# Optimization experiments

Hardware: AMD Instinct MI355X
Metric: run time of the kernel (lower is better)

## Reference

```python
import jax, jax.numpy as jnp
import numpy as np

E, N, R, OUT = 8, 4096, 128, 4096


def setup_inputs() -> dict:
    key = jax.random.key(0)
    kx, kw = jax.random.split(key)
    # x: stacked list of per-expert inputs, x[i] has shape [N, r]
    x = jax.random.normal(kx, (E, N, R), dtype=jnp.float32)
    # W: per-expert nn.Linear weights, torch layout [out_features, in_features]
    W = jax.random.normal(kw, (E, OUT, R), dtype=jnp.float32) * (1.0 / np.sqrt(R))
    return {"x": x, "W": W}


def reference(x, W):
    # Grouped GEMM over experts: out[e] = x[e] @ W[e].T  (Linear, no bias)
    # x: [E, N, r], W: [E, out, r] -> out: [E, N, out]
    return jnp.einsum("enr,eor->eno", x, W)
```

## Files before the change

### kernel.cpp

```cpp
#include <hip/hip_runtime.h>
#include <hip/hip_bf16.h>


#define NEXP 8
#define NROW 4096
#define KD   128
#define NOUT 4096
#define TILE 128

typedef __attribute__((ext_vector_type(8))) short bf16x8;
typedef __attribute__((ext_vector_type(4))) float f32x4;

__device__ __forceinline__ unsigned int pack2_bf16(float lo, float hi) {
  unsigned int ulo = __float_as_uint(lo);
  ulo += 0x7fffu + ((ulo >> 16) & 1u);
  unsigned int uhi = __float_as_uint(hi);
  uhi += 0x7fffu + ((uhi >> 16) & 1u);
  return (ulo >> 16) | (uhi & 0xffff0000u);
}

__global__ __launch_bounds__(512, 4)
void moe_gemm_bf16(const float* __restrict__ X, const float* __restrict__ W,
                   float* __restrict__ Out) {
  __shared__ unsigned short As[TILE * KD];
  __shared__ unsigned short Bs[TILE * KD];

  const int e    = blockIdx.z;
  const int row0 = blockIdx.y * TILE;
  const int col0 = blockIdx.x * TILE;
  const int t    = threadIdx.x;

  const float* xg = X + ((size_t)e * NROW + row0) * KD;
  const float* wg = W + ((size_t)e * NOUT + col0) * KD;

#pragma unroll
  for (int r = 0; r < 4; ++r) {
    const int flat = r * 4096 + t * 8;
    const int row  = flat >> 7;
    const int c    = (flat >> 3) & 15;
    const int cs   = c ^ (row & 15);
    const int lidx = row * KD + cs * 8;

    float4 a0 = *(const float4*)(xg + flat);
    float4 a1 = *(const float4*)(xg + flat + 4);
    float4 b0 = *(const float4*)(wg + flat);
    float4 b1 = *(const float4*)(wg + flat + 4);

    uint4 ap, bp;
    ap.x = pack2_bf16(a0.x, a0.y); ap.y = pack2_bf16(a0.z, a0.w);
    ap.z = pack2_bf16(a1.x, a1.y); ap.w = pack2_bf16(a1.z, a1.w);
    bp.x = pack2_bf16(b0.x, b0.y); bp.y = pack2_bf16(b0.z, b0.w);
    bp.z = pack2_bf16(b1.x, b1.y); bp.w = pack2_bf16(b1.z, b1.w);

    *(uint4*)(&As[lidx]) = ap;
    *(uint4*)(&Bs[lidx]) = bp;
  }
  __syncthreads();

  const int lane = t & 63;
  const int wave = t >> 6;
  const int quad = lane >> 4;
  const int l16  = lane & 15;
  const int wm   = (wave & 1) * 64;
  const int wn   = (wave >> 1) * 32;

  f32x4 acc[4][2];
#pragma unroll
  for (int i = 0; i < 4; ++i)
#pragma unroll
    for (int j = 0; j < 2; ++j)
      acc[i][j] = (f32x4)(0.0f);

#pragma unroll
  for (int ks = 0; ks < 4; ++ks) {
    const int c  = ks * 4 + quad;
    const int cs = c ^ l16;
    bf16x8 av[4], bv[2];
#pragma unroll
    for (int i = 0; i < 4; ++i) {
      const int row = wm + i * 16 + l16;
      av[i] = *(const bf16x8*)(&As[row * KD + cs * 8]);
    }
#pragma unroll
    for (int j = 0; j < 2; ++j) {
      const int row = wn + j * 16 + l16;
      bv[j] = *(const bf16x8*)(&Bs[row * KD + cs * 8]);
    }
#pragma unroll
    for (int i = 0; i < 4; ++i)
#pragma unroll
      for (int j = 0; j < 2; ++j)
        acc[i][j] = __builtin_amdgcn_mfma_f32_16x16x32_bf16(av[i], bv[j],
                                                            acc[i][j], 0, 0, 0);
  }

  float* og = Out + ((size_t)e * NROW + row0 + wm + quad * 4) * NOUT
                  + col0 + wn + l16;
#pragma unroll
  for (int i = 0; i < 4; ++i)
#pragma unroll
    for (int v = 0; v < 4; ++v) {
      float* orow = og + (size_t)(i * 16 + v) * NOUT;
#pragma unroll
      for (int j = 0; j < 2; ++j)
        __builtin_nontemporal_store(acc[i][j][v], orow + j * 16);
    }
}

extern "C" void kernel_launch(void* const* d_in, const int* in_sizes, int n_in,
                              void* d_out, int out_size, void* d_ws, size_t ws_size,
                              hipStream_t stream) {
  const float* X = (const float*)d_in[0];
  const float* W = (const float*)d_in[1];
  float* Out = (float*)d_out;
  dim3 grid(NOUT / TILE, NROW / TILE, NEXP);
  moe_gemm_bf16<<<grid, dim3(512, 1, 1), 0, stream>>>(X, W, Out);
}
```

Before: 595.4 us.

## Swap MFMA operands for vectorized float4 output stores and flatten grid by expert

The MFMA operands are swapped so each lane holds four consecutive output columns, which lets the epilogue write float4 nontemporal stores instead of scalar ones. The grid is also flattened to 1D with the expert index in the low bits, so consecutive workgroups spread across experts, which may interleave across XCDs. The kernel is dominated by the 512MB output write, and wider stores are meant to cut store instruction count and improve write coalescing. The expert interleaving may lower L2 reuse of the X and W tiles within an XCD.

```diff
diff --git a/kernel.cpp b/kernel.cpp
--- a/kernel.cpp
+++ b/kernel.cpp
@@ -25,13 +25,15 @@
   __shared__ unsigned short As[TILE * KD];
   __shared__ unsigned short Bs[TILE * KD];
 
-  const int e    = blockIdx.z;
-  const int row0 = blockIdx.y * TILE;
-  const int col0 = blockIdx.x * TILE;
+  const int wg   = blockIdx.x;
+  const int e    = wg & 7;
+  const int rem  = wg >> 3;
+  const int row0 = (rem >> 5) * TILE;
+  const int col0 = (rem & 31) * TILE;
   const int t    = threadIdx.x;
 
   const float* xg = X + ((size_t)e * NROW + row0) * KD;
-  const float* wg = W + ((size_t)e * NOUT + col0) * KD;
+  const float* wg_ = W + ((size_t)e * NOUT + col0) * KD;
 
 #pragma unroll
   for (int r = 0; r < 4; ++r) {
@@ -43,8 +45,8 @@
 
     float4 a0 = *(const float4*)(xg + flat);
     float4 a1 = *(const float4*)(xg + flat + 4);
-    float4 b0 = *(const float4*)(wg + flat);
-    float4 b1 = *(const float4*)(wg + flat + 4);
+    float4 b0 = *(const float4*)(wg_ + flat);
+    float4 b1 = *(const float4*)(wg_ + flat + 4);
 
     uint4 ap, bp;
     ap.x = pack2_bf16(a0.x, a0.y); ap.y = pack2_bf16(a0.z, a0.w);
@@ -90,21 +92,19 @@
     for (int i = 0; i < 4; ++i)
 #pragma unroll
       for (int j = 0; j < 2; ++j)
-        acc[i][j] = __builtin_amdgcn_mfma_f32_16x16x32_bf16(av[i], bv[j],
+        acc[i][j] = __builtin_amdgcn_mfma_f32_16x16x32_bf16(bv[j], av[i],
                                                             acc[i][j], 0, 0, 0);
   }
 
-  float* og = Out + ((size_t)e * NROW + row0 + wm + quad * 4) * NOUT
-                  + col0 + wn + l16;
+  float* og = Out + ((size_t)e * NROW + row0 + wm + l16) * NOUT
+                  + col0 + wn + quad * 4;
 #pragma unroll
-  for (int i = 0; i < 4; ++i)
+  for (int i = 0; i < 4; ++i) {
+    float* orow = og + (size_t)(i * 16) * NOUT;
 #pragma unroll
-    for (int v = 0; v < 4; ++v) {
-      float* orow = og + (size_t)(i * 16 + v) * NOUT;
-#pragma unroll
-      for (int j = 0; j < 2; ++j)
-        __builtin_nontemporal_store(acc[i][j][v], orow + j * 16);
-    }
+    for (int j = 0; j < 2; ++j)
+      __builtin_nontemporal_store(acc[i][j], (f32x4*)(orow + j * 16));
+  }
 }
 
 extern "C" void kernel_launch(void* const* d_in, const int* in_sizes, int n_in,
@@ -113,6 +113,6 @@
   const float* X = (const float*)d_in[0];
   const float* W = (const float*)d_in[1];
   float* Out = (float*)d_out;
-  dim3 grid(NOUT / TILE, NROW / TILE, NEXP);
+  dim3 grid(NEXP * (NROW / TILE) * (NOUT / TILE), 1, 1);
   moe_gemm_bf16<<<grid, dim3(512, 1, 1), 0, stream>>>(X, W, Out);
 }
```

Result: slower. 645.7 us (+8.5%).
